# Performance work log

Hardware: AMD Instinct MI355X
Metric: run time of the kernel (lower is better)

The kernel has to match this reference:

```python
import jax, jax.numpy as jnp
import numpy as np

IN_FEATURES = 4096
OUT_FEATURES = 4096
BATCH = 4096


def setup_inputs() -> dict:
    key = jax.random.key(0)
    ks = jax.random.split(key, 7)
    x = jax.random.normal(ks[0], (BATCH, IN_FEATURES), dtype=jnp.float32)
    # kaiming_normal fan_in with relu: std = sqrt(2/fan_in)
    weight_mu = jax.random.normal(ks[1], (OUT_FEATURES, IN_FEATURES), dtype=jnp.float32) * np.sqrt(2.0 / IN_FEATURES)
    # original init: uniform(-5.5, -2.5); use that range for realism
    weight_rho = jax.random.uniform(ks[2], (OUT_FEATURES, IN_FEATURES), dtype=jnp.float32, minval=-5.5, maxval=-2.5)
    bias_mu = jnp.zeros((OUT_FEATURES,), dtype=jnp.float32)
    bias_rho = jax.random.uniform(ks[3], (OUT_FEATURES,), dtype=jnp.float32, minval=-5.5, maxval=-2.5)
    weight_eps = jax.random.normal(ks[4], (OUT_FEATURES, IN_FEATURES), dtype=jnp.float32)
    bias_eps = jax.random.normal(ks[5], (OUT_FEATURES,), dtype=jnp.float32)
    return {
        "x": x,
        "weight_mu": weight_mu,
        "weight_rho": weight_rho,
        "bias_mu": bias_mu,
        "bias_rho": bias_rho,
        "weight_eps": weight_eps,
        "bias_eps": bias_eps,
    }


def reference(x, weight_mu, weight_rho, bias_mu, bias_rho, weight_eps, bias_eps):
    # sigma = softplus(rho) + 1e-8; sampled weight = mu + sigma * eps
    weight_sigma = jnp.log1p(jnp.exp(weight_rho)) + 1e-8
    bias_sigma = jnp.log1p(jnp.exp(bias_rho)) + 1e-8
    weight = weight_mu + weight_sigma * weight_eps  # [out, in]
    bias = bias_mu + bias_sigma * bias_eps          # [out]
    # F.linear(x, weight, bias) = x @ weight.T + bias
    return jnp.einsum("bi,oi->bo", x, weight) + bias
```

## Files before the change

kernel.cpp:

```cpp
#include <hip/hip_runtime.h>
#include <hip/hip_bf16.h>

typedef __bf16 bf16;
typedef __bf16 bf16x8 __attribute__((ext_vector_type(8)));
typedef float  f32x4  __attribute__((ext_vector_type(4)));

#define MDIM 4096
#define NDIM 4096
#define KDIM 4096
#define BM 128
#define BN 128
#define BK 32

__device__ __forceinline__ float softplus_eps(float r) {
    return log1pf(expf(r)) + 1e-8f;
}

__global__ void sample_weight_kernel(const float4* __restrict__ mu,
                                     const float4* __restrict__ rho,
                                     const float4* __restrict__ eps,
                                     ushort4* __restrict__ out, int n4) {
    int i = blockIdx.x * blockDim.x + threadIdx.x;
    if (i >= n4) return;
    float4 m = mu[i], r = rho[i], e = eps[i];
    float w0 = m.x + softplus_eps(r.x) * e.x;
    float w1 = m.y + softplus_eps(r.y) * e.y;
    float w2 = m.z + softplus_eps(r.z) * e.z;
    float w3 = m.w + softplus_eps(r.w) * e.w;
    ushort4 o;
    o.x = __builtin_bit_cast(unsigned short, (bf16)w0);
    o.y = __builtin_bit_cast(unsigned short, (bf16)w1);
    o.z = __builtin_bit_cast(unsigned short, (bf16)w2);
    o.w = __builtin_bit_cast(unsigned short, (bf16)w3);
    out[i] = o;
}

__global__ void cvt_x_kernel(const float4* __restrict__ x,
                             ushort4* __restrict__ out, int n4) {
    int i = blockIdx.x * blockDim.x + threadIdx.x;
    if (i >= n4) return;
    float4 v = x[i];
    ushort4 o;
    o.x = __builtin_bit_cast(unsigned short, (bf16)v.x);
    o.y = __builtin_bit_cast(unsigned short, (bf16)v.y);
    o.z = __builtin_bit_cast(unsigned short, (bf16)v.z);
    o.w = __builtin_bit_cast(unsigned short, (bf16)v.w);
    out[i] = o;
}

__global__ void sample_bias_kernel(const float* __restrict__ mu,
                                   const float* __restrict__ rho,
                                   const float* __restrict__ eps,
                                   float* __restrict__ out, int n) {
    int i = blockIdx.x * blockDim.x + threadIdx.x;
    if (i < n) out[i] = mu[i] + softplus_eps(rho[i]) * eps[i];
}

__device__ __forceinline__ void gload_lds16(const void* g, void* l) {
    __builtin_amdgcn_global_load_lds(
        (const __attribute__((address_space(1))) void*)g,
        (__attribute__((address_space(3))) void*)l, 16, 0, 0);
}

__global__ __launch_bounds__(256) void gemm_bt_kernel(const bf16* __restrict__ A,
                                                      const bf16* __restrict__ B,
                                                      const float* __restrict__ bias,
                                                      float* __restrict__ C) {
    __shared__ __align__(16) bf16 As[BM * BK];
    __shared__ __align__(16) bf16 Bs[BN * BK];

    const int nBN = NDIM / BN;
    const int cpx = (MDIM / BM) * nBN / 8;
    int bid = blockIdx.x;
    int swz = (bid & 7) * cpx + (bid >> 3);
    int bm = swz / nBN;
    int bn = swz % nBN;

    const int tid  = threadIdx.x;
    const int wave = tid >> 6;
    const int lane = tid & 63;
    const int wm = wave >> 1;
    const int wn = wave & 1;

    const int rowA = bm * BM + (tid >> 2);
    const int rowB = bn * BN + (tid >> 2);
    const int kofs = (tid & 3) * 8;
    const bf16* gA0 = A + rowA * KDIM + kofs;
    const bf16* gA1 = gA0 + 64 * KDIM;
    const bf16* gB0 = B + rowB * KDIM + kofs;
    const bf16* gB1 = gB0 + 64 * KDIM;
    const unsigned s0 = wave * 1024;
    const unsigned s1 = 4096 + wave * 1024;

    f32x4 acc[4][4] = {};

    const int rsel = lane & 15;
    const int ksel = (lane >> 4) * 8;

    for (int kb = 0; kb < KDIM; kb += BK) {
        gload_lds16(gA0 + kb, (char*)As + s0);
        gload_lds16(gA1 + kb, (char*)As + s1);
        gload_lds16(gB0 + kb, (char*)Bs + s0);
        gload_lds16(gB1 + kb, (char*)Bs + s1);
        __syncthreads();

        bf16x8 af[4], bfr[4];
        #pragma unroll
        for (int m = 0; m < 4; ++m)
            af[m] = *(const bf16x8*)&As[(wm * 64 + m * 16 + rsel) * BK + ksel];
        #pragma unroll
        for (int n = 0; n < 4; ++n)
            bfr[n] = *(const bf16x8*)&Bs[(wn * 64 + n * 16 + rsel) * BK + ksel];
        #pragma unroll
        for (int m = 0; m < 4; ++m)
            #pragma unroll
            for (int n = 0; n < 4; ++n)
                acc[m][n] = __builtin_amdgcn_mfma_f32_16x16x32_bf16(
                                af[m], bfr[n], acc[m][n], 0, 0, 0);
        __syncthreads();
    }

    #pragma unroll
    for (int n = 0; n < 4; ++n) {
        int gc = bn * BN + wn * 64 + n * 16 + (lane & 15);
        float bv = bias[gc];
        #pragma unroll
        for (int m = 0; m < 4; ++m) {
            int gr = bm * BM + wm * 64 + m * 16 + (lane >> 4) * 4;
            float* cp = C + gr * NDIM + gc;
            #pragma unroll
            for (int r = 0; r < 4; ++r)
                cp[r * NDIM] = acc[m][n][r] + bv;
        }
    }
}

extern "C" void kernel_launch(void* const* d_in, const int* in_sizes, int n_in,
                              void* d_out, int out_size, void* d_ws, size_t ws_size,
                              hipStream_t stream) {
    const float* x    = (const float*)d_in[0];
    const float* wmu  = (const float*)d_in[1];
    const float* wrho = (const float*)d_in[2];
    const float* bmu  = (const float*)d_in[3];
    const float* brho = (const float*)d_in[4];
    const float* weps = (const float*)d_in[5];
    const float* beps = (const float*)d_in[6];
    float* out = (float*)d_out;

    bf16*  w_bf = (bf16*)d_ws;
    bf16*  x_bf = (bf16*)((char*)d_ws + (size_t)NDIM * KDIM * 2);
    float* b_f  = (float*)((char*)d_ws + (size_t)NDIM * KDIM * 4);

    const int n4 = MDIM * KDIM / 4;
    sample_weight_kernel<<<n4 / 256, 256, 0, stream>>>(
        (const float4*)wmu, (const float4*)wrho, (const float4*)weps,
        (ushort4*)w_bf, n4);
    cvt_x_kernel<<<n4 / 256, 256, 0, stream>>>(
        (const float4*)x, (ushort4*)x_bf, n4);
    sample_bias_kernel<<<NDIM / 256, 256, 0, stream>>>(bmu, brho, beps, b_f, NDIM);

    gemm_bt_kernel<<<(MDIM / BM) * (NDIM / BN), 256, 0, stream>>>(x_bf, w_bf, b_f, out);
}
```

Baseline: 439.9 us.

## Replace GEMM with 256x256 8-wave ping-pong pipelined kernel using swizzled LDS

The bf16 GEMM kernel is replaced with a 256x256x64 tile kernel that runs 8 waves per block. It double-buffers LDS across two 64 KB slots, uses XOR-swizzled LDS chunks to avoid bank conflicts, and interleaves global-to-LDS loads with MFMA phases using barriers, vmcnt waits and s_setprio. The goal is to raise arithmetic intensity and hide memory latency compared with the single-buffered 128x128x32 kernel. In exchange it needs 128 KB of dynamic LDS with one block per CU, heavy register use, and a fragile hand-tuned schedule.

```diff
diff --git a/kernel.cpp b/kernel.cpp
--- a/kernel.cpp
+++ b/kernel.cpp
@@ -8,9 +8,6 @@
 #define MDIM 4096
 #define NDIM 4096
 #define KDIM 4096
-#define BM 128
-#define BN 128
-#define BK 32
 
 __device__ __forceinline__ float softplus_eps(float r) {
     return log1pf(expf(r)) + 1e-8f;
@@ -56,83 +53,187 @@
     if (i < n) out[i] = mu[i] + softplus_eps(rho[i]) * eps[i];
 }
 
-__device__ __forceinline__ void gload_lds16(const void* g, void* l) {
+__device__ __forceinline__ void gload_lds16(const bf16* g, char* l) {
     __builtin_amdgcn_global_load_lds(
         (const __attribute__((address_space(1))) void*)g,
         (__attribute__((address_space(3))) void*)l, 16, 0, 0);
 }
 
-__global__ __launch_bounds__(256) void gemm_bt_kernel(const bf16* __restrict__ A,
-                                                      const bf16* __restrict__ B,
-                                                      const float* __restrict__ bias,
-                                                      float* __restrict__ C) {
-    __shared__ __align__(16) bf16 As[BM * BK];
-    __shared__ __align__(16) bf16 Bs[BN * BK];
-
-    const int nBN = NDIM / BN;
-    const int cpx = (MDIM / BM) * nBN / 8;
+#define BAR()   __builtin_amdgcn_s_barrier()
+#define LGKM0() asm volatile("s_waitcnt lgkmcnt(0)" ::: "memory")
+#define VM6()   asm volatile("s_waitcnt vmcnt(6)" ::: "memory")
+#define PRIO(p) __builtin_amdgcn_s_setprio(p)
+#define mm(a, b, c) __builtin_amdgcn_mfma_f32_16x16x32_bf16((a), (b), (c), 0, 0, 0)
+
+__global__ __launch_bounds__(512, 1) void gemm8p_kernel(const bf16* __restrict__ A,
+                                                        const bf16* __restrict__ B,
+                                                        const float* __restrict__ bias,
+                                                        float* __restrict__ C) {
+    extern __shared__ __align__(16) char lds[];
+
+    const int tid  = threadIdx.x;
+    const int wave = tid >> 6, lane = tid & 63;
+    const int wm = wave >> 2, wn = wave & 3;
+    const int rsel = lane & 15, hi = lane >> 4;
+
     int bid = blockIdx.x;
-    int swz = (bid & 7) * cpx + (bid >> 3);
-    int bm = swz / nBN;
-    int bn = swz % nBN;
-
-    const int tid  = threadIdx.x;
-    const int wave = tid >> 6;
-    const int lane = tid & 63;
-    const int wm = wave >> 1;
-    const int wn = wave & 1;
-
-    const int rowA = bm * BM + (tid >> 2);
-    const int rowB = bn * BN + (tid >> 2);
-    const int kofs = (tid & 3) * 8;
-    const bf16* gA0 = A + rowA * KDIM + kofs;
-    const bf16* gA1 = gA0 + 64 * KDIM;
-    const bf16* gB0 = B + rowB * KDIM + kofs;
-    const bf16* gB1 = gB0 + 64 * KDIM;
-    const unsigned s0 = wave * 1024;
-    const unsigned s1 = 4096 + wave * 1024;
-
-    f32x4 acc[4][4] = {};
-
-    const int rsel = lane & 15;
-    const int ksel = (lane >> 4) * 8;
-
-    for (int kb = 0; kb < KDIM; kb += BK) {
-        gload_lds16(gA0 + kb, (char*)As + s0);
-        gload_lds16(gA1 + kb, (char*)As + s1);
-        gload_lds16(gB0 + kb, (char*)Bs + s0);
-        gload_lds16(gB1 + kb, (char*)Bs + s1);
-        __syncthreads();
-
-        bf16x8 af[4], bfr[4];
-        #pragma unroll
-        for (int m = 0; m < 4; ++m)
-            af[m] = *(const bf16x8*)&As[(wm * 64 + m * 16 + rsel) * BK + ksel];
-        #pragma unroll
-        for (int n = 0; n < 4; ++n)
-            bfr[n] = *(const bf16x8*)&Bs[(wn * 64 + n * 16 + rsel) * BK + ksel];
-        #pragma unroll
-        for (int m = 0; m < 4; ++m)
-            #pragma unroll
-            for (int n = 0; n < 4; ++n)
-                acc[m][n] = __builtin_amdgcn_mfma_f32_16x16x32_bf16(
-                                af[m], bfr[n], acc[m][n], 0, 0, 0);
-        __syncthreads();
+    int swz = (bid & 7) * 32 + (bid >> 3);
+    const int bm = swz >> 4, bn = swz & 15;
+
+    const int srow = tid >> 3;
+    const int sch  = ((tid & 7) ^ (srow & 7)) * 8;
+    const bf16* pA = A + (size_t)(bm * 256 + srow) * KDIM + sch;
+    const bf16* pB = B + (size_t)(bn * 256 + srow) * KDIM + sch;
+    char* ldsw = lds + wave * 1024;
+
+#define SLOT(s) ((s) * 65536)
+#define STAGE_A(t, s, h) do { \
+    gload_lds16(pA + (size_t)((h) * 128) * KDIM + (t) * 64,      ldsw + SLOT(s) + (h) * 16384); \
+    gload_lds16(pA + (size_t)((h) * 128 + 64) * KDIM + (t) * 64, ldsw + SLOT(s) + (h) * 16384 + 8192); } while (0)
+#define STAGE_B(t, s, h) do { \
+    gload_lds16(pB + (size_t)((h) * 128) * KDIM + (t) * 64,      ldsw + SLOT(s) + 32768 + (h) * 16384); \
+    gload_lds16(pB + (size_t)((h) * 128 + 64) * KDIM + (t) * 64, ldsw + SLOT(s) + 32768 + (h) * 16384 + 8192); } while (0)
+
+    const int cx  = rsel & 7;
+    const int ck0 = (hi ^ cx) * 16;
+    const int ck1 = ((hi + 4) ^ cx) * 16;
+    const int aBase = wm * 16384 + rsel * 128;
+    const int bBase = 32768 + wn * 8192 + rsel * 128;
+#define LDA(s, m, k) (*(const bf16x8*)(lds + SLOT(s) + aBase + (m) * 2048 + ((k) ? ck1 : ck0)))
+#define LDB(s, n, k) (*(const bf16x8*)(lds + SLOT(s) + bBase + (n) * 2048 + ((k) ? ck1 : ck0)))
+
+    f32x4 acc[8][4] = {};
+    bf16x8 rA0[4][2], rA1[4][2], rB[4][2];
+
+    STAGE_B(0, 0, 0); STAGE_B(0, 0, 1); STAGE_A(0, 0, 0); STAGE_A(0, 0, 1);
+    STAGE_B(1, 1, 0); STAGE_B(1, 1, 1); STAGE_A(1, 1, 0);
+    VM6();
+    BAR();
+
+    for (int i = 0; i < 32; ++i) {
+        const int t1 = (2 * i + 1) & 63, t2 = (2 * i + 2) & 63, t3 = (2 * i + 3) & 63;
+
+        #pragma unroll
+        for (int n = 0; n < 4; ++n) { rB[n][0] = LDB(0, n, 0); rB[n][1] = LDB(0, n, 1); }
+        #pragma unroll
+        for (int m = 0; m < 4; ++m) { rA0[m][0] = LDA(0, m, 0); rA0[m][1] = LDA(0, m, 1); }
+        STAGE_A(t1, 1, 1);
+        BAR(); LGKM0(); PRIO(1);
+        #pragma unroll
+        for (int m = 0; m < 4; ++m)
+            #pragma unroll
+            for (int n = 0; n < 2; ++n) {
+                acc[m][n] = mm(rA0[m][0], rB[n][0], acc[m][n]);
+                acc[m][n] = mm(rA0[m][1], rB[n][1], acc[m][n]);
+            }
+        PRIO(0); BAR();
+
+        #pragma unroll
+        for (int m = 0; m < 4; ++m) { rA1[m][0] = LDA(0, m + 4, 0); rA1[m][1] = LDA(0, m + 4, 1); }
+        STAGE_B(t2, 0, 0);
+        BAR(); LGKM0(); PRIO(1);
+        #pragma unroll
+        for (int m = 0; m < 4; ++m)
+            #pragma unroll
+            for (int n = 0; n < 2; ++n) {
+                acc[m + 4][n] = mm(rA1[m][0], rB[n][0], acc[m + 4][n]);
+                acc[m + 4][n] = mm(rA1[m][1], rB[n][1], acc[m + 4][n]);
+            }
+        PRIO(0); BAR();
+
+        STAGE_B(t2, 0, 1);
+        BAR(); LGKM0(); PRIO(1);
+        #pragma unroll
+        for (int m = 0; m < 4; ++m)
+            #pragma unroll
+            for (int n = 2; n < 4; ++n) {
+                acc[m + 4][n] = mm(rA1[m][0], rB[n][0], acc[m + 4][n]);
+                acc[m + 4][n] = mm(rA1[m][1], rB[n][1], acc[m + 4][n]);
+            }
+        PRIO(0); BAR();
+
+        STAGE_A(t2, 0, 0);
+        VM6();
+        BAR(); LGKM0(); PRIO(1);
+        #pragma unroll
+        for (int m = 0; m < 4; ++m)
+            #pragma unroll
+            for (int n = 2; n < 4; ++n) {
+                acc[m][n] = mm(rA0[m][0], rB[n][0], acc[m][n]);
+                acc[m][n] = mm(rA0[m][1], rB[n][1], acc[m][n]);
+            }
+        PRIO(0); BAR();
+
+        #pragma unroll
+        for (int n = 0; n < 4; ++n) { rB[n][0] = LDB(1, n, 0); rB[n][1] = LDB(1, n, 1); }
+        #pragma unroll
+        for (int m = 0; m < 4; ++m) { rA0[m][0] = LDA(1, m, 0); rA0[m][1] = LDA(1, m, 1); }
+        STAGE_A(t2, 0, 1);
+        BAR(); LGKM0(); PRIO(1);
+        #pragma unroll
+        for (int m = 0; m < 4; ++m)
+            #pragma unroll
+            for (int n = 0; n < 2; ++n) {
+                acc[m][n] = mm(rA0[m][0], rB[n][0], acc[m][n]);
+                acc[m][n] = mm(rA0[m][1], rB[n][1], acc[m][n]);
+            }
+        PRIO(0); BAR();
+
+        #pragma unroll
+        for (int m = 0; m < 4; ++m) { rA1[m][0] = LDA(1, m + 4, 0); rA1[m][1] = LDA(1, m + 4, 1); }
+        STAGE_B(t3, 1, 0);
+        BAR(); LGKM0(); PRIO(1);
+        #pragma unroll
+        for (int m = 0; m < 4; ++m)
+            #pragma unroll
+            for (int n = 0; n < 2; ++n) {
+                acc[m + 4][n] = mm(rA1[m][0], rB[n][0], acc[m + 4][n]);
+                acc[m + 4][n] = mm(rA1[m][1], rB[n][1], acc[m + 4][n]);
+            }
+        PRIO(0); BAR();
+
+        STAGE_B(t3, 1, 1);
+        BAR(); LGKM0(); PRIO(1);
+        #pragma unroll
+        for (int m = 0; m < 4; ++m)
+            #pragma unroll
+            for (int n = 2; n < 4; ++n) {
+                acc[m + 4][n] = mm(rA1[m][0], rB[n][0], acc[m + 4][n]);
+                acc[m + 4][n] = mm(rA1[m][1], rB[n][1], acc[m + 4][n]);
+            }
+        PRIO(0); BAR();
+
+        STAGE_A(t3, 1, 0);
+        VM6();
+        BAR(); LGKM0(); PRIO(1);
+        #pragma unroll
+        for (int m = 0; m < 4; ++m)
+            #pragma unroll
+            for (int n = 2; n < 4; ++n) {
+                acc[m][n] = mm(rA0[m][0], rB[n][0], acc[m][n]);
+                acc[m][n] = mm(rA0[m][1], rB[n][1], acc[m][n]);
+            }
+        PRIO(0); BAR();
     }
 
     #pragma unroll
     for (int n = 0; n < 4; ++n) {
-        int gc = bn * BN + wn * 64 + n * 16 + (lane & 15);
-        float bv = bias[gc];
-        #pragma unroll
-        for (int m = 0; m < 4; ++m) {
-            int gr = bm * BM + wm * 64 + m * 16 + (lane >> 4) * 4;
-            float* cp = C + gr * NDIM + gc;
+        const int gc = bn * 256 + wn * 64 + n * 16 + rsel;
+        const float bv = bias[gc];
+        #pragma unroll
+        for (int m = 0; m < 8; ++m) {
+            const int gr = bm * 256 + wm * 128 + m * 16 + hi * 4;
+            float* cp = C + (size_t)gr * NDIM + gc;
             #pragma unroll
             for (int r = 0; r < 4; ++r)
-                cp[r * NDIM] = acc[m][n][r] + bv;
+                cp[(size_t)r * NDIM] = acc[m][n][r] + bv;
         }
     }
+#undef SLOT
+#undef STAGE_A
+#undef STAGE_B
+#undef LDA
+#undef LDB
 }
 
 extern "C" void kernel_launch(void* const* d_in, const int* in_sizes, int n_in,
@@ -159,5 +260,7 @@
         (const float4*)x, (ushort4*)x_bf, n4);
     sample_bias_kernel<<<NDIM / 256, 256, 0, stream>>>(bmu, brho, beps, b_f, NDIM);
 
-    gemm_bt_kernel<<<(MDIM / BM) * (NDIM / BN), 256, 0, stream>>>(x_bf, w_bf, b_f, out);
-}
+    hipFuncSetAttribute((const void*)gemm8p_kernel,
+                        hipFuncAttributeMaxDynamicSharedMemorySize, 131072);
+    gemm8p_kernel<<<(MDIM / 256) * (NDIM / 256), 512, 131072, stream>>>(x_bf, w_bf, b_f, out);
+}
```

After: 378.1 us. 14.0% less time.
